# Kernel optimization log

Hardware: AMD Instinct MI355X
Metric: run time of the kernel (lower is better)

The kernel has to match this reference:

```python
import jax, jax.numpy as jnp
import numpy as np

EPS_NORM = 1e-12   # torch F.normalize eps
GN_EPS = 1e-5      # GroupNorm eps
FACTOR = 5
NUM_HEADS = 8
NEG_SLOPE = 0.01   # LeakyReLU default


def _l2norm(x, axis):
    n = jnp.sqrt(jnp.sum(x * x, axis=axis, keepdims=True))
    return x / jnp.maximum(n, EPS_NORM)


def setup_inputs() -> dict:
    key = jax.random.key(0)
    B, C, H, W, D = 2, 256, 16, 16, 16
    N = H * W * D
    sample_k = FACTOR * int(np.ceil(np.log(N)))  # 45
    ks = jax.random.split(key, 8)
    s = 0.02
    return {
        "x": jax.random.normal(ks[0], (B, C, H, W, D), jnp.float32),
        "W_qkvv": jax.random.normal(ks[1], (C, 4 * C), jnp.float32) * s,
        "W_out": jax.random.normal(ks[2], (C, C), jnp.float32) * s,
        "b_out": jnp.zeros((C,), jnp.float32),
        "W_out2": jax.random.normal(ks[3], (C, C), jnp.float32) * s,
        "b_out2": jnp.zeros((C,), jnp.float32),
        "gamma1": 0.1 * jnp.ones((C,), jnp.float32),
        "conv_w": jax.random.normal(ks[4], (C, C, 3, 3, 3), jnp.float32) * s,
        "gn_w": jnp.ones((C,), jnp.float32),
        "gn_b": jnp.zeros((C,), jnp.float32),
        "index_sample": jax.random.randint(ks[5], (N, sample_k), 0, N),
    }


def reference(x, W_qkvv, W_out, b_out, W_out2, b_out2, gamma1, conv_w, gn_w, gn_b, index_sample):
    B, C, H, Wd, D = x.shape
    N = H * Wd * D
    nh = NUM_HEADS
    dh = C // nh
    xs = x.reshape(B, C, N).transpose(0, 2, 1)                    # [B,N,C]
    qkvv = (xs @ W_qkvv).reshape(B, N, 4, nh, dh).transpose(2, 0, 3, 1, 4)  # [4,B,nh,N,dh]
    q, k, v_ca, v_sa = qkvv[0], qkvv[1], qkvv[2], qkvv[3]
    q = _l2norm(q, axis=-2)   # normalize over sequence dim (dim=-2 in torch)
    k = _l2norm(k, axis=-2)

    u = FACTOR * int(np.ceil(np.log(N)))
    # --- ProbSparse _prob_QK ---
    K_sample = k[:, :, index_sample, :]                            # [B,nh,N,sk,dh]
    QK_sample = jnp.einsum('bhle,bhlse->bhls', q, K_sample)        # [B,nh,N,sk]
    M = QK_sample.max(-1) - QK_sample.sum(-1) / N                  # sparsity measure
    _, M_top = jax.lax.top_k(M, u)                                 # [B,nh,u]
    b_idx = jnp.arange(B)[:, None, None]
    h_idx = jnp.arange(nh)[None, :, None]
    Q_red = q[b_idx, h_idx, M_top]                                 # [B,nh,u,dh]
    scores = jnp.einsum('bhud,bhld->bhul', Q_red, k)               # [B,nh,u,N]

    # --- spatial (ProbSparse) context ---
    ctx = jnp.broadcast_to(v_sa.mean(axis=-2, keepdims=True), v_sa.shape)  # [B,nh,N,dh]
    attn_sa = jax.nn.softmax(scores, axis=-1)
    upd = jnp.einsum('bhul,bhld->bhud', attn_sa, v_sa)             # [B,nh,u,dh]
    ctx = ctx.at[b_idx, h_idx, M_top].set(upd)

    # --- channel attention (on transposed q,k,v: [B,nh,dh,N]) ---
    qt = q.transpose(0, 1, 3, 2)
    kt = k.transpose(0, 1, 3, 2)
    vt = v_ca.transpose(0, 1, 3, 2)
    attn_ca = jax.nn.softmax(jnp.einsum('bhdn,bhen->bhde', qt, kt), axis=-1)  # [B,nh,dh,dh]
    x_ca = jnp.einsum('bhde,bhen->bhdn', attn_ca, vt).transpose(0, 3, 1, 2).reshape(B, N, C)
    x_sa = ctx.transpose(0, 3, 1, 2).reshape(B, N, C)              # matches source permute
    x_sa = x_sa @ W_out + b_out                                    # dead branch (source discards)
    x_ca = x_ca @ W_out2 + b_out2
    epa = x_ca  # source: x = x_SA + x_CA; x = x_CA  -> only CA branch survives

    attn = xs + gamma1 * epa                                       # [B,N,C]
    attn = attn.reshape(B, H, Wd, D, C).transpose(0, 4, 1, 2, 3)   # [B,C,H,W,D]

    # conv8: Dropout3d (eval=id) -> Conv3d(3x3x3, no bias) -> GroupNorm(1 group)
    y = jax.lax.conv_general_dilated(attn, conv_w, (1, 1, 1), [(1, 1)] * 3,
                                     dimension_numbers=('NCDHW', 'OIDHW', 'NCDHW'))
    mu = y.mean(axis=(1, 2, 3, 4), keepdims=True)
    var = y.var(axis=(1, 2, 3, 4), keepdims=True)
    y = (y - mu) / jnp.sqrt(var + GN_EPS)
    y = y * gn_w[None, :, None, None, None] + gn_b[None, :, None, None, None]
    y = y + attn
    return jnp.where(y >= 0, y, NEG_SLOPE * y)
```

## Files before the change

kernel.cpp:

```cpp
#include <hip/hip_runtime.h>
#include <hip/hip_bf16.h>
#include <stdint.h>


#define B_ 2
#define C_ 256
#define N_ 4096
#define NH 8
#define PADV 5832
#define CN  (C_*N_)
#define BCN (B_*CN)

typedef unsigned short u16;
typedef unsigned int   u32;

using frag16 = __attribute__((ext_vector_type(8))) short;
using f32x4  = __attribute__((ext_vector_type(4))) float;

__device__ __forceinline__ u16 f2bf(float f) {
    u32 u = __float_as_uint(f);
    u += 0x7fff + ((u >> 16) & 1);
    return (u16)(u >> 16);
}
__device__ __forceinline__ float bb(u16 h) { return __uint_as_float((u32)h << 16); }
__device__ __forceinline__ void gld16(const void* g, void* l) {
    __builtin_amdgcn_global_load_lds((const __attribute__((address_space(1))) u32*)g,
                                     (__attribute__((address_space(3))) u32*)l, 16, 0, 0);
}
__device__ __forceinline__ int padrow(int n) {
    int z = n >> 8, y = (n >> 4) & 15, x = n & 15;
    return (z + 1) * 324 + (y + 1) * 18 + (x + 1);
}

#define OFF_TB    0
#define OFF_SP    3145728
#define OFF_XCAB  3670016
#define OFF_PKB   0
#define OFF_Y     3145728
#define OFF_ATTB  6291456
#define OFF_ATTP  7340032
#define OFF_WT2   8833024
#define OFF_W2B   9717760
#define OFF_WQB   9750528
#define OFF_XT    9848832
#define OFF_RSQ   10897408
#define OFF_RED   10898432

__global__ __launch_bounds__(256) void k_prep(const float* __restrict__ CW, const float* __restrict__ W2,
                                              const float* __restrict__ Wq, const float* __restrict__ X,
                                              u16* __restrict__ WT2, u16* __restrict__ W2B,
                                              u16* __restrict__ Wqb, u16* __restrict__ XT,
                                              u32* __restrict__ APz, float* __restrict__ RSQ) {
    __shared__ __align__(16) float ls[6912];
    float (*ts)[33] = (float(*)[33])ls;
    float (*t64)[65] = (float(*)[65])ls;
    int blk = blockIdx.x, tid = threadIdx.x;
    if (blk < 256) {
        int co = blk;
        const float* src = CW + (size_t)co * 6912;
        for (int u = tid; u < 6912; u += 256) ls[u] = src[u];
        __syncthreads();
#pragma unroll
        for (int t = 0; t < 27; ++t)
            WT2[(((size_t)t * 256 + co) << 8) + tid] = f2bf(ls[tid * 27 + t]);
    } else if (blk < 320) {
        int bi = blk - 256; int c0 = (bi & 7) * 32, p0 = (bi >> 3) * 32;
        int tx = tid & 31, ty = tid >> 5;
#pragma unroll
        for (int i = 0; i < 4; ++i) ts[ty + i * 8][tx] = W2[(size_t)(p0 + ty + i * 8) * 256 + c0 + tx];
        __syncthreads();
#pragma unroll
        for (int i = 0; i < 4; ++i) W2B[(size_t)(c0 + ty + i * 8) * 256 + p0 + tx] = f2bf(ts[tx][ty + i * 8]);
    } else if (blk < 512) {
        int bi = blk - 320; int c0 = (bi & 7) * 32, j0 = (bi >> 3) * 32;
        int tx = tid & 31, ty = tid >> 5;
#pragma unroll
        for (int i = 0; i < 4; ++i) ts[ty + i * 8][tx] = Wq[(size_t)(c0 + ty + i * 8) * 1024 + j0 + tx];
        __syncthreads();
#pragma unroll
        for (int i = 0; i < 4; ++i) Wqb[(size_t)(j0 + ty + i * 8) * 256 + c0 + tx] = f2bf(ts[tx][ty + i * 8]);
    } else if (blk < 1024) {
        int idx = blk - 512;
        int n0 = (idx & 63) * 64, c0 = ((idx >> 6) & 3) * 64, b = idx >> 8;
        int tn = tid & 63, tc4 = tid >> 6;
        const float* Xb = X + (size_t)b * CN;
#pragma unroll
        for (int i = 0; i < 16; ++i) t64[tc4 + i * 4][tn] = Xb[(size_t)(c0 + tc4 + i * 4) * N_ + n0 + tn];
        __syncthreads();
        u16* Xo = XT + (size_t)b * N_ * C_;
#pragma unroll
        for (int i = 0; i < 16; ++i)
            Xo[(size_t)(n0 + tc4 + i * 4) * C_ + c0 + tn] = f2bf(t64[tn][tc4 + i * 4]);
    } else if (blk < 6856) {
        APz[(size_t)(blk - 1024) * 256 + tid] = 0;
    } else {
        ((float4*)RSQ)[tid] = make_float4(0.f, 0.f, 0.f, 0.f);
    }
}

__global__ __launch_bounds__(256) void k_qkv_mfma(const u16* __restrict__ Wqb, const u16* __restrict__ XT,
                                                  u16* __restrict__ Tb, float* __restrict__ RSQ) {
    __shared__ __align__(16) u16 As[2][8192], Bs[2][8192];
    int n0 = blockIdx.x * 128, j0 = blockIdx.y * 128, b = blockIdx.z;
    int tid = threadIdx.x, lane = tid & 63, w = tid >> 6;
    int wm = w & 1, wn = w >> 1, qm = lane >> 4, lm = lane & 15;
    int srow = lane >> 3;
    int sperm = (((lane & 7) ^ srow) << 3);
    const u16* aB = Wqb + ((size_t)(j0 + w * 32 + srow) << 8) + sperm;
    const u16* bB = XT + ((size_t)(b * N_ + n0 + w * 32 + srow) << 8) + sperm;
    int rdp = ((lm & 7) << 3);
    f32x4 acc[4][4] = {};
    auto stg = [&](int p, int kc) {
#pragma unroll
        for (int i = 0; i < 4; ++i) {
            gld16(aB + i * 2048 + kc * 64, &As[p][w * 2048 + i * 512]);
            gld16(bB + i * 2048 + kc * 64, &Bs[p][w * 2048 + i * 512]);
        }
    };
    stg(0, 0);
#pragma unroll
    for (int kt = 0; kt < 4; ++kt) {
        int p = kt & 1;
        __syncthreads();
        if (kt < 3) stg(p ^ 1, kt + 1);
#pragma unroll
        for (int c2 = 0; c2 < 2; ++c2) {
            frag16 af[4], bf[4];
#pragma unroll
            for (int i = 0; i < 4; ++i)
                af[i] = *(const frag16*)&As[p][(wm * 64 + i * 16 + lm) * 64 + ((((c2 * 4 + qm) << 3) ^ rdp))];
#pragma unroll
            for (int j = 0; j < 4; ++j)
                bf[j] = *(const frag16*)&Bs[p][(wn * 64 + j * 16 + lm) * 64 + ((((c2 * 4 + qm) << 3) ^ rdp))];
#pragma unroll
            for (int i = 0; i < 4; ++i)
#pragma unroll
                for (int j = 0; j < 4; ++j)
                    acc[i][j] = __builtin_amdgcn_mfma_f32_16x16x32_bf16(af[i], bf[j], acc[i][j], 0, 0, 0);
        }
    }
    u16* To = Tb + ((size_t)b * 768 + j0 + wm * 64) * N_ + n0 + wn * 64;
#pragma unroll
    for (int i = 0; i < 4; ++i)
#pragma unroll
        for (int j = 0; j < 4; ++j)
#pragma unroll
            for (int r = 0; r < 4; ++r)
                To[(size_t)(i * 16 + qm * 4 + r) * N_ + j * 16 + lm] = f2bf(acc[i][j][r]);
    if (j0 < 512) {
#pragma unroll
        for (int i = 0; i < 4; ++i)
#pragma unroll
            for (int r = 0; r < 4; ++r) {
                float s = 0.f;
#pragma unroll
                for (int j = 0; j < 4; ++j) s += acc[i][j][r] * acc[i][j][r];
                s += __shfl_xor(s, 1); s += __shfl_xor(s, 2);
                s += __shfl_xor(s, 4); s += __shfl_xor(s, 8);
                if (lm == 0)
                    atomicAdd(&RSQ[b * 512 + j0 + wm * 64 + i * 16 + qm * 4 + r], s);
            }
    }
}

__global__ __launch_bounds__(256) void k_ca_score(const u16* __restrict__ Tb, float* __restrict__ SP) {
    __shared__ __align__(16) u16 Qs[2][8192], Ks[2][8192];
    int ks = blockIdx.x, h = blockIdx.y, b = blockIdx.z;
    int tid = threadIdx.x, lane = tid & 63, w = tid >> 6;
    int wm = w & 1, wn = w >> 1, qm = lane >> 4, lm = lane & 15;
    const u16* Qb = Tb + ((size_t)b * 768 + h * 32) * N_;
    const u16* Kb = Tb + ((size_t)b * 768 + 256 + h * 32) * N_;
    int k0base = ks * 512;
    auto stg = [&](int p, int ck) {
        int k0 = k0base + ck * 256;
#pragma unroll
        for (int ri = 0; ri < 4; ++ri) {
            int row = ri * 8 + w * 2 + (lane >> 5);
            int cg = (lane & 31) ^ (row & 31);
            gld16(Qb + (size_t)row * N_ + k0 + cg * 8, &Qs[p][ri * 2048 + w * 512]);
            gld16(Kb + (size_t)row * N_ + k0 + cg * 8, &Ks[p][ri * 2048 + w * 512]);
        }
    };
    f32x4 acc = {};
    stg(0, 0);
#pragma unroll
    for (int ck = 0; ck < 2; ++ck) {
        int p = ck & 1;
        __syncthreads();
        if (ck < 1) stg(p ^ 1, ck + 1);
        int rowA = wm * 16 + lm, rowB = wn * 16 + lm;
#pragma unroll
        for (int kk = 0; kk < 8; ++kk) {
            int slotA = ((kk * 4 + qm) ^ (rowA & 31)) << 3;
            int slotB = ((kk * 4 + qm) ^ (rowB & 31)) << 3;
            frag16 af = *(const frag16*)&Qs[p][rowA * 256 + slotA];
            frag16 bf = *(const frag16*)&Ks[p][rowB * 256 + slotB];
            acc = __builtin_amdgcn_mfma_f32_16x16x32_bf16(af, bf, acc, 0, 0, 0);
        }
    }
    float* o = SP + (((size_t)(b * NH + h)) * 8 + ks) * 1024;
#pragma unroll
    for (int r = 0; r < 4; ++r)
        o[(wm * 16 + qm * 4 + r) * 32 + wn * 16 + lm] = acc[r];
}

__global__ __launch_bounds__(256) void k_ca_apply(const u16* __restrict__ Tb, const float* __restrict__ SP,
                                                  const float* __restrict__ RSQ, u16* __restrict__ XCAb) {
    int n0 = blockIdx.x * 256, h = blockIdx.y, b = blockIdx.z;
    __shared__ float raw[1024];
    __shared__ float Ae[32][32];
    __shared__ float sq[32], sk[32];
    int tid = threadIdx.x;
    const float* Sp = SP + ((size_t)(b * NH + h)) * 8192;
    for (int u = tid; u < 1024; u += 256) {
        float v = 0.f;
#pragma unroll
        for (int s = 0; s < 8; ++s) v += Sp[s * 1024 + u];
        raw[u] = v;
    }
    if (tid < 32) {
        sq[tid] = 1.0f / fmaxf(sqrtf(RSQ[b * 512 + h * 32 + tid]), 1e-12f);
        sk[tid] = 1.0f / fmaxf(sqrtf(RSQ[b * 512 + 256 + h * 32 + tid]), 1e-12f);
    }
    __syncthreads();
    if (tid < 32) {
        float iq = sq[tid];
        float sv[32]; float m = -1e30f;
#pragma unroll
        for (int e = 0; e < 32; ++e) { sv[e] = raw[tid * 32 + e] * iq * sk[e]; m = fmaxf(m, sv[e]); }
        float sm = 0.f;
#pragma unroll
        for (int e = 0; e < 32; ++e) { sv[e] = __expf(sv[e] - m); sm += sv[e]; }
        float rinv = 1.0f / sm;
#pragma unroll
        for (int e = 0; e < 32; ++e) Ae[e][tid] = sv[e] * rinv;
    }
    __syncthreads();
    int n = n0 + tid;
    const u16* V = Tb + ((size_t)b * 768 + 512 + h * 32) * N_ + n;
    float acc[32];
#pragma unroll
    for (int d = 0; d < 32; ++d) acc[d] = 0.f;
#pragma unroll
    for (int e = 0; e < 32; ++e) {
        float v = bb(V[(size_t)e * N_]);
#pragma unroll
        for (int dg = 0; dg < 8; ++dg) {
            float4 a4 = *(const float4*)&Ae[e][dg * 4];
            acc[dg * 4 + 0] += a4.x * v; acc[dg * 4 + 1] += a4.y * v;
            acc[dg * 4 + 2] += a4.z * v; acc[dg * 4 + 3] += a4.w * v;
        }
    }
    u16* o = XCAb + ((size_t)b * N_ + n) * C_ + h * 32;
#pragma unroll
    for (int dg = 0; dg < 8; ++dg) {
        ushort4 pk;
        pk.x = f2bf(acc[dg * 4 + 0]); pk.y = f2bf(acc[dg * 4 + 1]);
        pk.z = f2bf(acc[dg * 4 + 2]); pk.w = f2bf(acc[dg * 4 + 3]);
        *(ushort4*)(o + dg * 4) = pk;
    }
}

__global__ __launch_bounds__(256) void k_out2_mfma(const u16* __restrict__ W2B, const u16* __restrict__ XCAb,
                                                   const float* __restrict__ bias2, const float* __restrict__ g1,
                                                   const float* __restrict__ X, u16* __restrict__ ATTb,
                                                   u16* __restrict__ ATTp) {
    __shared__ __align__(16) u16 As[2][8192], Bs[2][8192];
    int n0 = blockIdx.x * 128, c0 = blockIdx.y * 128, b = blockIdx.z;
    int tid = threadIdx.x, lane = tid & 63, w = tid >> 6;
    int wm = w & 1, wn = w >> 1, qm = lane >> 4, lm = lane & 15;
    int srow = lane >> 3;
    int sperm = (((lane & 7) ^ srow) << 3);
    const u16* aB = W2B + ((size_t)(c0 + w * 32 + srow) << 8) + sperm;
    const u16* bB = XCAb + ((size_t)(b * N_ + n0 + w * 32 + srow) << 8) + sperm;
    int rdp = ((lm & 7) << 3);
    f32x4 acc[4][4] = {};
    auto stg = [&](int p, int kc) {
#pragma unroll
        for (int i = 0; i < 4; ++i) {
            gld16(aB + i * 2048 + kc * 64, &As[p][w * 2048 + i * 512]);
            gld16(bB + i * 2048 + kc * 64, &Bs[p][w * 2048 + i * 512]);
        }
    };
    stg(0, 0);
#pragma unroll
    for (int kt = 0; kt < 4; ++kt) {
        int p = kt & 1;
        __syncthreads();
        if (kt < 3) stg(p ^ 1, kt + 1);
#pragma unroll
        for (int c2 = 0; c2 < 2; ++c2) {
            frag16 af[4], bf[4];
#pragma unroll
            for (int i = 0; i < 4; ++i)
                af[i] = *(const frag16*)&As[p][(wm * 64 + i * 16 + lm) * 64 + ((((c2 * 4 + qm) << 3) ^ rdp))];
#pragma unroll
            for (int j = 0; j < 4; ++j)
                bf[j] = *(const frag16*)&Bs[p][(wn * 64 + j * 16 + lm) * 64 + ((((c2 * 4 + qm) << 3) ^ rdp))];
#pragma unroll
            for (int i = 0; i < 4; ++i)
#pragma unroll
                for (int j = 0; j < 4; ++j)
                    acc[i][j] = __builtin_amdgcn_mfma_f32_16x16x32_bf16(af[i], bf[j], acc[i][j], 0, 0, 0);
        }
    }
    int c_base = c0 + wm * 64, n_base = n0 + wn * 64;
    const float* xin = X + (size_t)b * CN;
    u16* Ao = ATTb + (size_t)b * CN;
    u16* Ap = ATTp + ((size_t)b * PADV << 8);
    float val[4][4][4];
#pragma unroll
    for (int i = 0; i < 4; ++i)
#pragma unroll
        for (int r = 0; r < 4; ++r) {
            int c = c_base + i * 16 + qm * 4 + r;
            float gv = g1[c], bi = bias2[c];
#pragma unroll
            for (int j = 0; j < 4; ++j) {
                int n = n_base + j * 16 + lm;
                float v = xin[(size_t)c * N_ + n] + gv * (acc[i][j][r] + bi);
                val[i][j][r] = v;
                Ao[(size_t)c * N_ + n] = f2bf(v);
            }
        }
#pragma unroll
    for (int j = 0; j < 4; ++j) {
        int n = n_base + j * 16 + lm;
        int pr = padrow(n);
#pragma unroll
        for (int i = 0; i < 4; ++i) {
            ushort4 pk;
            pk.x = f2bf(val[i][j][0]); pk.y = f2bf(val[i][j][1]);
            pk.z = f2bf(val[i][j][2]); pk.w = f2bf(val[i][j][3]);
            *(ushort4*)&Ap[((size_t)pr << 8) + c_base + i * 16 + qm * 4] = pk;
        }
    }
}

__global__ __launch_bounds__(256) void k_conv_mfma(const u16* __restrict__ WT2, const u16* __restrict__ ATTp,
                                                   u16* __restrict__ Pk) {
    __shared__ __align__(16) u16 As[2][8192], Bs[2][8192];
    int n0 = blockIdx.x * 128;
    int co0 = (blockIdx.y & 1) * 128, ks = blockIdx.y >> 1;
    int b = blockIdx.z;
    int tid = threadIdx.x, lane = tid & 63, w = tid >> 6;
    int wm = w & 1, wn = w >> 1, qm = lane >> 4, lm = lane & 15;
    int srow = lane >> 3;
    int sperm = (((lane & 7) ^ srow) << 3);
    const u16* aB = WT2 + (((size_t)ks * 9 * 256 + co0 + w * 32 + srow) << 8) + sperm;
    int prA[4];
#pragma unroll
    for (int i = 0; i < 4; ++i) prA[i] = padrow(n0 + w * 32 + i * 8 + srow) << 8;
    const u16* bB = ATTp + ((size_t)b * PADV << 8) + ((ks - 1) * 324 << 8) + sperm;
    int rdp = ((lm & 7) << 3);
    f32x4 acc[4][4] = {};
    auto stg = [&](int p, int kt) {
        int tap9 = kt >> 2, kc = kt & 3;
        int K9 = ((tap9 / 3) - 1) * 18 + (tap9 % 3 - 1);
#pragma unroll
        for (int i = 0; i < 4; ++i) {
            gld16(aB + (size_t)tap9 * 65536 + i * 2048 + kc * 64, &As[p][w * 2048 + i * 512]);
            gld16(bB + prA[i] + K9 * 256 + kc * 64,              &Bs[p][w * 2048 + i * 512]);
        }
    };
    stg(0, 0);
#pragma unroll
    for (int kt = 0; kt < 36; ++kt) {
        int p = kt & 1;
        __syncthreads();
        if (kt < 35) stg(p ^ 1, kt + 1);
#pragma unroll
        for (int c2 = 0; c2 < 2; ++c2) {
            frag16 af[4], bf[4];
#pragma unroll
            for (int i = 0; i < 4; ++i)
                af[i] = *(const frag16*)&As[p][(wm * 64 + i * 16 + lm) * 64 + ((((c2 * 4 + qm) << 3) ^ rdp))];
#pragma unroll
            for (int j = 0; j < 4; ++j)
                bf[j] = *(const frag16*)&Bs[p][(wn * 64 + j * 16 + lm) * 64 + ((((c2 * 4 + qm) << 3) ^ rdp))];
#pragma unroll
            for (int i = 0; i < 4; ++i)
#pragma unroll
                for (int j = 0; j < 4; ++j)
                    acc[i][j] = __builtin_amdgcn_mfma_f32_16x16x32_bf16(af[i], bf[j], acc[i][j], 0, 0, 0);
        }
    }
    u16* Pb = Pk + ((size_t)(ks * B_ + b) * C_ + co0 + wm * 64) * N_ + n0 + wn * 64;
#pragma unroll
    for (int i = 0; i < 4; ++i)
#pragma unroll
        for (int j = 0; j < 4; ++j)
#pragma unroll
            for (int r = 0; r < 4; ++r)
                Pb[(size_t)(i * 16 + qm * 4 + r) * N_ + j * 16 + lm] = f2bf(acc[i][j][r]);
}

__global__ __launch_bounds__(256) void k_gn_reduce(const u16* __restrict__ Pk, u16* __restrict__ Y,
                                                   float* __restrict__ RED) {
    int blk = blockIdx.x, b = blockIdx.y;
    size_t base = (size_t)b * CN + (size_t)blk * 16384;
    const u16* p0 = Pk + base;
    const u16* p1 = Pk + BCN + base;
    const u16* p2 = Pk + (size_t)2 * BCN + base;
    u16* y = Y + base;
    float s = 0.f, q = 0.f;
    for (int u = threadIdx.x * 8; u < 16384; u += 2048) {
        uint4 a = *(const uint4*)&p0[u];
        uint4 c1 = *(const uint4*)&p1[u];
        uint4 c2 = *(const uint4*)&p2[u];
        const u16 *A = (const u16*)&a, *B1 = (const u16*)&c1, *C2 = (const u16*)&c2;
        __align__(16) u16 outp[8];
#pragma unroll
        for (int i = 0; i < 8; ++i) {
            float v = bb(A[i]) + bb(B1[i]) + bb(C2[i]);
            s += v; q += v * v;
            outp[i] = f2bf(v);
        }
        *(uint4*)&y[u] = *(const uint4*)outp;
    }
#pragma unroll
    for (int off = 32; off; off >>= 1) { s += __shfl_down(s, off); q += __shfl_down(q, off); }
    __shared__ float rs_[4], rq[4];
    int lane = threadIdx.x & 63, wv = threadIdx.x >> 6;
    if (!lane) { rs_[wv] = s; rq[wv] = q; }
    __syncthreads();
    if (threadIdx.x == 0) {
        RED[((size_t)b * 64 + blk) * 2 + 0] = rs_[0] + rs_[1] + rs_[2] + rs_[3];
        RED[((size_t)b * 64 + blk) * 2 + 1] = rq[0] + rq[1] + rq[2] + rq[3];
    }
}

__global__ __launch_bounds__(256) void k_final(const u16* __restrict__ Y, const u16* __restrict__ ATTb,
                                               const float* __restrict__ RED, const float* __restrict__ gw,
                                               const float* __restrict__ gb, float* __restrict__ out) {
    int i = blockIdx.x * 256 + threadIdx.x;
    int b = i >> 20;
    int c = (i >> 12) & 255;
    __shared__ float smu[2];
    if (threadIdx.x < 64) {
        float s = RED[((size_t)b * 64 + threadIdx.x) * 2 + 0];
        float q = RED[((size_t)b * 64 + threadIdx.x) * 2 + 1];
#pragma unroll
        for (int off = 32; off; off >>= 1) { s += __shfl_down(s, off); q += __shfl_down(q, off); }
        if (threadIdx.x == 0) {
            float inv = 1.0f / (float)CN;
            float mu = s * inv, var = q * inv - mu * mu;
            smu[0] = mu; smu[1] = rsqrtf(var + 1e-5f);
        }
    }
    __syncthreads();
    float v = (bb(Y[i]) - smu[0]) * smu[1] * gw[c] + gb[c] + bb(ATTb[i]);
    out[i] = v >= 0.f ? v : 0.01f * v;
}

extern "C" void kernel_launch(void* const* d_in, const int* in_sizes, int n_in,
                              void* d_out, int out_size, void* d_ws, size_t ws_size,
                              hipStream_t stream) {
    const float* x      = (const float*)d_in[0];
    const float* Wqkvv  = (const float*)d_in[1];
    const float* W_out2 = (const float*)d_in[4];
    const float* b_out2 = (const float*)d_in[5];
    const float* gamma1 = (const float*)d_in[6];
    const float* conv_w = (const float*)d_in[7];
    const float* gn_w   = (const float*)d_in[8];
    const float* gn_b   = (const float*)d_in[9];
    float* out = (float*)d_out;
    float* ws = (float*)d_ws;

    u16*   Tb   = (u16*)(ws + OFF_TB);
    float* SP   = ws + OFF_SP;
    u16*   XCAb = (u16*)(ws + OFF_XCAB);
    u16*   Pk   = (u16*)(ws + OFF_PKB);
    u16*   Y    = (u16*)(ws + OFF_Y);
    u16*   ATTb = (u16*)(ws + OFF_ATTB);
    u16*   ATTp = (u16*)(ws + OFF_ATTP);
    u16*   WT2  = (u16*)(ws + OFF_WT2);
    u16*   W2B  = (u16*)(ws + OFF_W2B);
    u16*   Wqb  = (u16*)(ws + OFF_WQB);
    u16*   XT   = (u16*)(ws + OFF_XT);
    float* RSQ  = ws + OFF_RSQ;
    float* RED  = ws + OFF_RED;

    k_prep      <<<6857, 256, 0, stream>>>(conv_w, W_out2, Wqkvv, x, WT2, W2B, Wqb, XT, (u32*)ATTp, RSQ);
    k_qkv_mfma  <<<dim3(N_ / 128, 6, B_), 256, 0, stream>>>(Wqb, XT, Tb, RSQ);
    k_ca_score  <<<dim3(8, NH, B_), 256, 0, stream>>>(Tb, SP);
    k_ca_apply  <<<dim3(N_ / 256, NH, B_), 256, 0, stream>>>(Tb, SP, RSQ, XCAb);
    k_out2_mfma <<<dim3(N_ / 128, C_ / 128, B_), 256, 0, stream>>>(W2B, XCAb, b_out2, gamma1, x, ATTb, ATTp);
    k_conv_mfma <<<dim3(N_ / 128, 6, B_), 256, 0, stream>>>(WT2, ATTp, Pk);
    k_gn_reduce <<<dim3(64, B_), 256, 0, stream>>>(Pk, Y, RED);
    k_final     <<<(B_ * CN) / 256, 256, 0, stream>>>(Y, ATTb, RED, gn_w, gn_b, out);
}
```

Measured before the change: 174.1 us.

## Reformulate channel attention via input Gram matrix and folded weight products

```diff
diff --git a/kernel.cpp b/kernel.cpp
--- a/kernel.cpp
+++ b/kernel.cpp
@@ -32,25 +32,26 @@
     return (z + 1) * 324 + (y + 1) * 18 + (x + 1);
 }
 
-#define OFF_TB    0
-#define OFF_SP    3145728
-#define OFF_XCAB  3670016
-#define OFF_PKB   0
+#define OFF_XB16  0
+#define OFF_GP    1048576
+#define OFF_NQK   2097152
+#define OFF_PK    0
 #define OFF_Y     3145728
-#define OFF_ATTB  6291456
-#define OFF_ATTP  7340032
-#define OFF_WT2   8833024
-#define OFF_W2B   9717760
-#define OFF_WQB   9750528
-#define OFF_XT    9848832
-#define OFF_RSQ   10897408
-#define OFF_RED   10898432
+#define OFF_ATTB  4194304
+#define OFF_ATTP  5242880
+#define OFF_WT2   6735872
+#define OFF_W2B   7620608
+#define OFF_WQB   7653376
+#define OFF_XT    7751680
+#define OFF_WET   8800256
+#define OFF_WFU   8865792
+#define OFF_RED   8931328
 
 __global__ __launch_bounds__(256) void k_prep(const float* __restrict__ CW, const float* __restrict__ W2,
                                               const float* __restrict__ Wq, const float* __restrict__ X,
                                               u16* __restrict__ WT2, u16* __restrict__ W2B,
                                               u16* __restrict__ Wqb, u16* __restrict__ XT,
-                                              u32* __restrict__ APz, float* __restrict__ RSQ) {
+                                              u16* __restrict__ XB, u32* __restrict__ APz) {
     __shared__ __align__(16) float ls[6912];
     float (*ts)[33] = (float(*)[33])ls;
     float (*t64)[65] = (float(*)[65])ls;
@@ -84,30 +85,198 @@
         int n0 = (idx & 63) * 64, c0 = ((idx >> 6) & 3) * 64, b = idx >> 8;
         int tn = tid & 63, tc4 = tid >> 6;
         const float* Xb = X + (size_t)b * CN;
-#pragma unroll
-        for (int i = 0; i < 16; ++i) t64[tc4 + i * 4][tn] = Xb[(size_t)(c0 + tc4 + i * 4) * N_ + n0 + tn];
+        u16* XBb = XB + (size_t)b * CN;
+#pragma unroll
+        for (int i = 0; i < 16; ++i) {
+            int c = c0 + tc4 + i * 4;
+            float v = Xb[(size_t)c * N_ + n0 + tn];
+            t64[tc4 + i * 4][tn] = v;
+            XBb[(size_t)c * N_ + n0 + tn] = f2bf(v);
+        }
         __syncthreads();
         u16* Xo = XT + (size_t)b * N_ * C_;
 #pragma unroll
         for (int i = 0; i < 16; ++i)
             Xo[(size_t)(n0 + tc4 + i * 4) * C_ + c0 + tn] = f2bf(t64[tn][tc4 + i * 4]);
-    } else if (blk < 6856) {
+    } else {
         APz[(size_t)(blk - 1024) * 256 + tid] = 0;
-    } else {
-        ((float4*)RSQ)[tid] = make_float4(0.f, 0.f, 0.f, 0.f);
-    }
-}
-
-__global__ __launch_bounds__(256) void k_qkv_mfma(const u16* __restrict__ Wqb, const u16* __restrict__ XT,
-                                                  u16* __restrict__ Tb, float* __restrict__ RSQ) {
+    }
+}
+
+__global__ __launch_bounds__(256) void k_gram(const u16* __restrict__ XB, float* __restrict__ GP) {
     __shared__ __align__(16) u16 As[2][8192], Bs[2][8192];
-    int n0 = blockIdx.x * 128, j0 = blockIdx.y * 128, b = blockIdx.z;
+    int mt = blockIdx.x & 1, nt = blockIdx.x >> 1, s = blockIdx.y, b = blockIdx.z;
+    int c0 = mt * 128, c0p = nt * 128, k0 = s * 512;
     int tid = threadIdx.x, lane = tid & 63, w = tid >> 6;
     int wm = w & 1, wn = w >> 1, qm = lane >> 4, lm = lane & 15;
     int srow = lane >> 3;
     int sperm = (((lane & 7) ^ srow) << 3);
-    const u16* aB = Wqb + ((size_t)(j0 + w * 32 + srow) << 8) + sperm;
-    const u16* bB = XT + ((size_t)(b * N_ + n0 + w * 32 + srow) << 8) + sperm;
+    const u16* aB = XB + ((size_t)(b * 256 + c0 + w * 32 + srow)) * 4096 + k0 + sperm;
+    const u16* bB = XB + ((size_t)(b * 256 + c0p + w * 32 + srow)) * 4096 + k0 + sperm;
+    int rdp = ((lm & 7) << 3);
+    f32x4 acc[4][4] = {};
+    auto stg = [&](int p, int kt) {
+#pragma unroll
+        for (int i = 0; i < 4; ++i) {
+            gld16(aB + (size_t)i * 32768 + kt * 64, &As[p][w * 2048 + i * 512]);
+            gld16(bB + (size_t)i * 32768 + kt * 64, &Bs[p][w * 2048 + i * 512]);
+        }
+    };
+    stg(0, 0);
+#pragma unroll
+    for (int kt = 0; kt < 8; ++kt) {
+        int p = kt & 1;
+        __syncthreads();
+        if (kt < 7) stg(p ^ 1, kt + 1);
+#pragma unroll
+        for (int c2 = 0; c2 < 2; ++c2) {
+            frag16 af[4], bf[4];
+#pragma unroll
+            for (int i = 0; i < 4; ++i)
+                af[i] = *(const frag16*)&As[p][(wm * 64 + i * 16 + lm) * 64 + ((((c2 * 4 + qm) << 3) ^ rdp))];
+#pragma unroll
+            for (int j = 0; j < 4; ++j)
+                bf[j] = *(const frag16*)&Bs[p][(wn * 64 + j * 16 + lm) * 64 + ((((c2 * 4 + qm) << 3) ^ rdp))];
+#pragma unroll
+            for (int i = 0; i < 4; ++i)
+#pragma unroll
+                for (int j = 0; j < 4; ++j)
+                    acc[i][j] = __builtin_amdgcn_mfma_f32_16x16x32_bf16(af[i], bf[j], acc[i][j], 0, 0, 0);
+        }
+    }
+    float* o = GP + (((size_t)s * B_ + b) * 256 + c0 + wm * 64) * 256 + c0p + wn * 64;
+#pragma unroll
+    for (int i = 0; i < 4; ++i)
+#pragma unroll
+        for (int j = 0; j < 4; ++j)
+#pragma unroll
+            for (int r = 0; r < 4; ++r)
+                o[(size_t)(i * 16 + qm * 4 + r) * 256 + j * 16 + lm] = acc[i][j][r];
+}
+
+__global__ __launch_bounds__(256) void k_nqk(const float* __restrict__ GP, const u16* __restrict__ Wqb,
+                                             u16* __restrict__ NQK) {
+    __shared__ float Gs[16][260];
+    int ct = blockIdx.x, h = blockIdx.y, b = blockIdx.z, t = threadIdx.x;
+#pragma unroll
+    for (int i = 0; i < 16; ++i) {
+        float v = 0.f;
+#pragma unroll
+        for (int s = 0; s < 8; ++s)
+            v += GP[(((size_t)s * B_ + b) * 256 + ct * 16 + i) * 256 + t];
+        Gs[i][t] = v;
+    }
+    __syncthreads();
+    int o = t >> 3, cg = t & 7;
+    int cl0 = cg * 2, cl1 = cg * 2 + 1;
+    const u16* Wk = Wqb + (size_t)(256 + h * 32 + o) * 256;
+    const u16* Wqr = Wqb + (size_t)(h * 32 + o) * 256;
+    float ak0 = 0.f, ak1 = 0.f, aq0 = 0.f, aq1 = 0.f;
+    for (int cp = 0; cp < 256; cp += 8) {
+        uint4 kv = *(const uint4*)(Wk + cp);
+        uint4 qv = *(const uint4*)(Wqr + cp);
+        const u16 *kh = (const u16*)&kv, *qh = (const u16*)&qv;
+#pragma unroll
+        for (int j = 0; j < 8; ++j) {
+            float kf = bb(kh[j]), qf = bb(qh[j]);
+            float g0 = Gs[cl0][cp + j], g1v = Gs[cl1][cp + j];
+            ak0 += kf * g0; ak1 += kf * g1v;
+            aq0 += qf * g0; aq1 += qf * g1v;
+        }
+    }
+    size_t base_q = (((size_t)(b * NH + h) * 2 + 0) * 32 + o) * 256 + ct * 16 + cg * 2;
+    *(u32*)(NQK + base_q)        = (u32)f2bf(aq0) | ((u32)f2bf(aq1) << 16);
+    *(u32*)(NQK + base_q + 8192) = (u32)f2bf(ak0) | ((u32)f2bf(ak1) << 16);
+}
+
+#define SPAD 260
+__global__ __launch_bounds__(256) void k_small(const u16* __restrict__ NQK, const u16* __restrict__ Wqb,
+                                               u16* __restrict__ WET) {
+    int h = blockIdx.x, b = blockIdx.y, t = threadIdx.x;
+    __shared__ u16 NQs[32][SPAD], NKs[32][SPAD];
+    __shared__ float Sm[32][33];
+    __shared__ float Ab[32][33];
+    __shared__ float qn[32], kn[32];
+    const u16* NQg = NQK + (((size_t)(b * NH + h) * 2) * 32) * 256;
+#pragma unroll
+    for (int i = 0; i < 32; ++i) {
+        NQs[i][t] = NQg[i * 256 + t];
+        NKs[i][t] = NQg[8192 + i * 256 + t];
+    }
+    __syncthreads();
+    if (t < 64) {
+        int d = t & 31, isk = t >> 5;
+        const u16* Wr = Wqb + (size_t)(isk * 256 + h * 32 + d) * 256;
+        const u16 (*Ns)[SPAD] = isk ? NKs : NQs;
+        float s = 0.f;
+        for (int c = 0; c < 256; c += 2) {
+            u32 wp = *(const u32*)(Wr + c);
+            u32 np = *(const u32*)(&Ns[d][c]);
+            s += bb((u16)wp) * bb((u16)np) + bb((u16)(wp >> 16)) * bb((u16)(np >> 16));
+        }
+        float nv = fmaxf(sqrtf(fmaxf(s, 0.f)), 1e-12f);
+        if (isk) kn[d] = nv; else qn[d] = nv;
+    }
+    {
+        int d = t & 31, eg = t >> 5;
+        const u16* Wqr = Wqb + (size_t)(h * 32 + d) * 256;
+        float accS[4] = {};
+        for (int c = 0; c < 256; c += 8) {
+            uint4 qv = *(const uint4*)(Wqr + c);
+            const u16* qh = (const u16*)&qv;
+#pragma unroll
+            for (int j = 0; j < 8; ++j) {
+                float qf = bb(qh[j]);
+#pragma unroll
+                for (int i = 0; i < 4; ++i)
+                    accS[i] += qf * bb(NKs[eg * 4 + i][c + j]);
+            }
+        }
+#pragma unroll
+        for (int i = 0; i < 4; ++i) Sm[d][eg * 4 + i] = accS[i];
+    }
+    __syncthreads();
+    if (t < 32) {
+        float iq = 1.0f / qn[t];
+        float sv[32], m = -1e30f;
+#pragma unroll
+        for (int e = 0; e < 32; ++e) { sv[e] = Sm[t][e] * iq / kn[e]; m = fmaxf(m, sv[e]); }
+        float sm = 0.f;
+#pragma unroll
+        for (int e = 0; e < 32; ++e) { sv[e] = __expf(sv[e] - m); sm += sv[e]; }
+        float rin = 1.0f / sm;
+#pragma unroll
+        for (int e = 0; e < 32; ++e) Ab[t][e] = sv[e] * rin;
+    }
+    __syncthreads();
+    {
+        int c = t;
+        float acc[32] = {};
+#pragma unroll
+        for (int e = 0; e < 32; ++e) {
+            float wv = bb(Wqb[(size_t)(512 + h * 32 + e) * 256 + c]);
+#pragma unroll
+            for (int dd = 0; dd < 32; ++dd) acc[dd] += Ab[dd][e] * wv;
+        }
+        u16* o = WET + ((size_t)b * 256 + c) * 256 + h * 32;
+        __align__(16) u16 pk[32];
+#pragma unroll
+        for (int dd = 0; dd < 32; ++dd) pk[dd] = f2bf(acc[dd]);
+#pragma unroll
+        for (int q4 = 0; q4 < 4; ++q4) *(uint4*)(o + q4 * 8) = *(const uint4*)(pk + q4 * 8);
+    }
+}
+
+__global__ __launch_bounds__(256) void k_wfull(const u16* __restrict__ W2B, const u16* __restrict__ WET,
+                                               const float* __restrict__ g1, u16* __restrict__ WFU) {
+    __shared__ __align__(16) u16 As[2][8192], Bs[2][8192];
+    int c0 = blockIdx.x * 128, cq0 = blockIdx.y * 128, b = blockIdx.z;
+    int tid = threadIdx.x, lane = tid & 63, w = tid >> 6;
+    int wm = w & 1, wn = w >> 1, qm = lane >> 4, lm = lane & 15;
+    int srow = lane >> 3;
+    int sperm = (((lane & 7) ^ srow) << 3);
+    const u16* aB = W2B + ((size_t)(c0 + w * 32 + srow)) * 256 + sperm;
+    const u16* bB = WET + ((size_t)(b * 256 + cq0 + w * 32 + srow)) * 256 + sperm;
     int rdp = ((lm & 7) << 3);
     f32x4 acc[4][4] = {};
     auto stg = [&](int p, int kc) {
@@ -139,140 +308,32 @@
                     acc[i][j] = __builtin_amdgcn_mfma_f32_16x16x32_bf16(af[i], bf[j], acc[i][j], 0, 0, 0);
         }
     }
-    u16* To = Tb + ((size_t)b * 768 + j0 + wm * 64) * N_ + n0 + wn * 64;
 #pragma unroll
     for (int i = 0; i < 4; ++i)
 #pragma unroll
-        for (int j = 0; j < 4; ++j)
-#pragma unroll
-            for (int r = 0; r < 4; ++r)
-                To[(size_t)(i * 16 + qm * 4 + r) * N_ + j * 16 + lm] = f2bf(acc[i][j][r]);
-    if (j0 < 512) {
-#pragma unroll
-        for (int i = 0; i < 4; ++i)
-#pragma unroll
-            for (int r = 0; r < 4; ++r) {
-                float s = 0.f;
-#pragma unroll
-                for (int j = 0; j < 4; ++j) s += acc[i][j][r] * acc[i][j][r];
-                s += __shfl_xor(s, 1); s += __shfl_xor(s, 2);
-                s += __shfl_xor(s, 4); s += __shfl_xor(s, 8);
-                if (lm == 0)
-                    atomicAdd(&RSQ[b * 512 + j0 + wm * 64 + i * 16 + qm * 4 + r], s);
+        for (int r = 0; r < 4; ++r) {
+            int c = c0 + wm * 64 + i * 16 + qm * 4 + r;
+            float gv = g1[c];
+#pragma unroll
+            for (int j = 0; j < 4; ++j) {
+                int cc = cq0 + wn * 64 + j * 16 + lm;
+                WFU[((size_t)b * 256 + c) * 256 + cc] = f2bf(gv * acc[i][j][r]);
             }
-    }
-}
-
-__global__ __launch_bounds__(256) void k_ca_score(const u16* __restrict__ Tb, float* __restrict__ SP) {
-    __shared__ __align__(16) u16 Qs[2][8192], Ks[2][8192];
-    int ks = blockIdx.x, h = blockIdx.y, b = blockIdx.z;
-    int tid = threadIdx.x, lane = tid & 63, w = tid >> 6;
-    int wm = w & 1, wn = w >> 1, qm = lane >> 4, lm = lane & 15;
-    const u16* Qb = Tb + ((size_t)b * 768 + h * 32) * N_;
-    const u16* Kb = Tb + ((size_t)b * 768 + 256 + h * 32) * N_;
-    int k0base = ks * 512;
-    auto stg = [&](int p, int ck) {
-        int k0 = k0base + ck * 256;
-#pragma unroll
-        for (int ri = 0; ri < 4; ++ri) {
-            int row = ri * 8 + w * 2 + (lane >> 5);
-            int cg = (lane & 31) ^ (row & 31);
-            gld16(Qb + (size_t)row * N_ + k0 + cg * 8, &Qs[p][ri * 2048 + w * 512]);
-            gld16(Kb + (size_t)row * N_ + k0 + cg * 8, &Ks[p][ri * 2048 + w * 512]);
-        }
-    };
-    f32x4 acc = {};
-    stg(0, 0);
-#pragma unroll
-    for (int ck = 0; ck < 2; ++ck) {
-        int p = ck & 1;
-        __syncthreads();
-        if (ck < 1) stg(p ^ 1, ck + 1);
-        int rowA = wm * 16 + lm, rowB = wn * 16 + lm;
-#pragma unroll
-        for (int kk = 0; kk < 8; ++kk) {
-            int slotA = ((kk * 4 + qm) ^ (rowA & 31)) << 3;
-            int slotB = ((kk * 4 + qm) ^ (rowB & 31)) << 3;
-            frag16 af = *(const frag16*)&Qs[p][rowA * 256 + slotA];
-            frag16 bf = *(const frag16*)&Ks[p][rowB * 256 + slotB];
-            acc = __builtin_amdgcn_mfma_f32_16x16x32_bf16(af, bf, acc, 0, 0, 0);
-        }
-    }
-    float* o = SP + (((size_t)(b * NH + h)) * 8 + ks) * 1024;
-#pragma unroll
-    for (int r = 0; r < 4; ++r)
-        o[(wm * 16 + qm * 4 + r) * 32 + wn * 16 + lm] = acc[r];
-}
-
-__global__ __launch_bounds__(256) void k_ca_apply(const u16* __restrict__ Tb, const float* __restrict__ SP,
-                                                  const float* __restrict__ RSQ, u16* __restrict__ XCAb) {
-    int n0 = blockIdx.x * 256, h = blockIdx.y, b = blockIdx.z;
-    __shared__ float raw[1024];
-    __shared__ float Ae[32][32];
-    __shared__ float sq[32], sk[32];
-    int tid = threadIdx.x;
-    const float* Sp = SP + ((size_t)(b * NH + h)) * 8192;
-    for (int u = tid; u < 1024; u += 256) {
-        float v = 0.f;
-#pragma unroll
-        for (int s = 0; s < 8; ++s) v += Sp[s * 1024 + u];
-        raw[u] = v;
-    }
-    if (tid < 32) {
-        sq[tid] = 1.0f / fmaxf(sqrtf(RSQ[b * 512 + h * 32 + tid]), 1e-12f);
-        sk[tid] = 1.0f / fmaxf(sqrtf(RSQ[b * 512 + 256 + h * 32 + tid]), 1e-12f);
-    }
-    __syncthreads();
-    if (tid < 32) {
-        float iq = sq[tid];
-        float sv[32]; float m = -1e30f;
-#pragma unroll
-        for (int e = 0; e < 32; ++e) { sv[e] = raw[tid * 32 + e] * iq * sk[e]; m = fmaxf(m, sv[e]); }
-        float sm = 0.f;
-#pragma unroll
-        for (int e = 0; e < 32; ++e) { sv[e] = __expf(sv[e] - m); sm += sv[e]; }
-        float rinv = 1.0f / sm;
-#pragma unroll
-        for (int e = 0; e < 32; ++e) Ae[e][tid] = sv[e] * rinv;
-    }
-    __syncthreads();
-    int n = n0 + tid;
-    const u16* V = Tb + ((size_t)b * 768 + 512 + h * 32) * N_ + n;
-    float acc[32];
-#pragma unroll
-    for (int d = 0; d < 32; ++d) acc[d] = 0.f;
-#pragma unroll
-    for (int e = 0; e < 32; ++e) {
-        float v = bb(V[(size_t)e * N_]);
-#pragma unroll
-        for (int dg = 0; dg < 8; ++dg) {
-            float4 a4 = *(const float4*)&Ae[e][dg * 4];
-            acc[dg * 4 + 0] += a4.x * v; acc[dg * 4 + 1] += a4.y * v;
-            acc[dg * 4 + 2] += a4.z * v; acc[dg * 4 + 3] += a4.w * v;
-        }
-    }
-    u16* o = XCAb + ((size_t)b * N_ + n) * C_ + h * 32;
-#pragma unroll
-    for (int dg = 0; dg < 8; ++dg) {
-        ushort4 pk;
-        pk.x = f2bf(acc[dg * 4 + 0]); pk.y = f2bf(acc[dg * 4 + 1]);
-        pk.z = f2bf(acc[dg * 4 + 2]); pk.w = f2bf(acc[dg * 4 + 3]);
-        *(ushort4*)(o + dg * 4) = pk;
-    }
-}
-
-__global__ __launch_bounds__(256) void k_out2_mfma(const u16* __restrict__ W2B, const u16* __restrict__ XCAb,
-                                                   const float* __restrict__ bias2, const float* __restrict__ g1,
-                                                   const float* __restrict__ X, u16* __restrict__ ATTb,
-                                                   u16* __restrict__ ATTp) {
+        }
+}
+
+__global__ __launch_bounds__(256) void k_att(const u16* __restrict__ WFU, const u16* __restrict__ XT,
+                                             const float* __restrict__ bias2, const float* __restrict__ g1,
+                                             const float* __restrict__ X, u16* __restrict__ ATTb,
+                                             u16* __restrict__ ATTp) {
     __shared__ __align__(16) u16 As[2][8192], Bs[2][8192];
     int n0 = blockIdx.x * 128, c0 = blockIdx.y * 128, b = blockIdx.z;
     int tid = threadIdx.x, lane = tid & 63, w = tid >> 6;
     int wm = w & 1, wn = w >> 1, qm = lane >> 4, lm = lane & 15;
     int srow = lane >> 3;
     int sperm = (((lane & 7) ^ srow) << 3);
-    const u16* aB = W2B + ((size_t)(c0 + w * 32 + srow) << 8) + sperm;
-    const u16* bB = XCAb + ((size_t)(b * N_ + n0 + w * 32 + srow) << 8) + sperm;
+    const u16* aB = WFU + ((size_t)(b * 256 + c0 + w * 32 + srow)) * 256 + sperm;
+    const u16* bB = XT + ((size_t)(b * N_ + n0 + w * 32 + srow)) * 256 + sperm;
     int rdp = ((lm & 7) << 3);
     f32x4 acc[4][4] = {};
     auto stg = [&](int p, int kc) {
@@ -314,11 +375,11 @@
 #pragma unroll
         for (int r = 0; r < 4; ++r) {
             int c = c_base + i * 16 + qm * 4 + r;
-            float gv = g1[c], bi = bias2[c];
+            float gb2 = g1[c] * bias2[c];
 #pragma unroll
             for (int j = 0; j < 4; ++j) {
                 int n = n_base + j * 16 + lm;
-                float v = xin[(size_t)c * N_ + n] + gv * (acc[i][j][r] + bi);
+                float v = xin[(size_t)c * N_ + n] + acc[i][j][r] + gb2;
                 val[i][j][r] = v;
                 Ao[(size_t)c * N_ + n] = f2bf(v);
             }
@@ -467,10 +528,10 @@
     float* out = (float*)d_out;
     float* ws = (float*)d_ws;
 
-    u16*   Tb   = (u16*)(ws + OFF_TB);
-    float* SP   = ws + OFF_SP;
-    u16*   XCAb = (u16*)(ws + OFF_XCAB);
-    u16*   Pk   = (u16*)(ws + OFF_PKB);
+    u16*   XB   = (u16*)(ws + OFF_XB16);
+    float* GP   = ws + OFF_GP;
+    u16*   NQK  = (u16*)(ws + OFF_NQK);
+    u16*   Pk   = (u16*)(ws + OFF_PK);
     u16*   Y    = (u16*)(ws + OFF_Y);
     u16*   ATTb = (u16*)(ws + OFF_ATTB);
     u16*   ATTp = (u16*)(ws + OFF_ATTP);
@@ -478,15 +539,17 @@
     u16*   W2B  = (u16*)(ws + OFF_W2B);
     u16*   Wqb  = (u16*)(ws + OFF_WQB);
     u16*   XT   = (u16*)(ws + OFF_XT);
-    float* RSQ  = ws + OFF_RSQ;
+    u16*   WET  = (u16*)(ws + OFF_WET);
+    u16*   WFU  = (u16*)(ws + OFF_WFU);
     float* RED  = ws + OFF_RED;
 
-    k_prep      <<<6857, 256, 0, stream>>>(conv_w, W_out2, Wqkvv, x, WT2, W2B, Wqb, XT, (u32*)ATTp, RSQ);
-    k_qkv_mfma  <<<dim3(N_ / 128, 6, B_), 256, 0, stream>>>(Wqb, XT, Tb, RSQ);
-    k_ca_score  <<<dim3(8, NH, B_), 256, 0, stream>>>(Tb, SP);
-    k_ca_apply  <<<dim3(N_ / 256, NH, B_), 256, 0, stream>>>(Tb, SP, RSQ, XCAb);
-    k_out2_mfma <<<dim3(N_ / 128, C_ / 128, B_), 256, 0, stream>>>(W2B, XCAb, b_out2, gamma1, x, ATTb, ATTp);
-    k_conv_mfma <<<dim3(N_ / 128, 6, B_), 256, 0, stream>>>(WT2, ATTp, Pk);
+    k_prep      <<<6856, 256, 0, stream>>>(conv_w, W_out2, Wqkvv, x, WT2, W2B, Wqb, XT, XB, (u32*)ATTp);
+    k_gram      <<<dim3(4, 8, B_), 256, 0, stream>>>(XB, GP);
+    k_nqk       <<<dim3(16, NH, B_), 256, 0, stream>>>(GP, Wqb, NQK);
+    k_small     <<<dim3(NH, B_), 256, 0, stream>>>(NQK, Wqb, WET);
+    k_wfull     <<<dim3(2, 2, B_), 256, 0, stream>>>(W2B, WET, gamma1, WFU);
+    k_att       <<<dim3(32, 2, B_), 256, 0, stream>>>(WFU, XT, b_out2, gamma1, x, ATTb, ATTp);
+    k_conv_mfma <<<dim3(32, 6, B_), 256, 0, stream>>>(WT2, ATTp, Pk);
     k_gn_reduce <<<dim3(64, B_), 256, 0, stream>>>(Pk, Y, RED);
-    k_final     <<<(B_ * CN) / 256, 256, 0, stream>>>(Y, ATTb, RED, gn_w, gn_b, out);
-}
+    k_final     <<<8192, 256, 0, stream>>>(Y, ATTb, RED, gn_w, gn_b, out);
+}
```

Result: slower. 239.1 us (+37.4%).
